# Performance work log

Hardware: AMD Instinct MI355X
Metric: run time of the kernel (lower is better)

## Reference

```python
import jax, jax.numpy as jnp
import numpy as np

N = 100000
E = 1600000
C_IN = 128
C_OUT = 128
EPS = 1e-5


def setup_inputs() -> dict:
    key = jax.random.key(0)
    ks = jax.random.split(key, 8)
    x = jax.random.normal(ks[0], (N, C_IN), dtype=jnp.float32)
    edge_index = jax.random.randint(ks[1], (2, E), 0, N, dtype=jnp.int64)
    s_proj = 1.0 / np.sqrt(C_IN)
    s_out = 1.0 / np.sqrt(C_IN)
    W_proj = jax.random.uniform(ks[2], (C_IN, C_IN), jnp.float32, -s_proj, s_proj)
    b_proj = jax.random.uniform(ks[3], (C_IN,), jnp.float32, -s_proj, s_proj)
    W_l = jax.random.uniform(ks[4], (C_OUT, C_IN), jnp.float32, -s_out, s_out)
    b_l = jax.random.uniform(ks[5], (C_OUT,), jnp.float32, -s_out, s_out)
    W_r = jax.random.uniform(ks[6], (C_OUT, C_IN), jnp.float32, -s_out, s_out)
    gamma = jnp.ones((C_OUT,), jnp.float32)
    beta = jnp.zeros((C_OUT,), jnp.float32)
    return {"x": x, "edge_index": edge_index, "W_proj": W_proj, "b_proj": b_proj,
            "W_l": W_l, "b_l": b_l, "W_r": W_r, "gamma": gamma, "beta": beta}


def reference(x, edge_index, W_proj, b_proj, W_l, b_l, W_r, gamma, beta):
    # SAGEConv(project=True, aggr='sum'): project+ReLU source features per node,
    # gather along edges, scatter-sum at targets, then lin_l(agg) + lin_r(x_root).
    src, dst = edge_index[0], edge_index[1]
    h = jax.nn.relu(x @ W_proj.T + b_proj)            # [N, C_IN]
    msg = h[src]                                       # [E, C_IN] edge gather
    agg = jax.ops.segment_sum(msg, dst, num_segments=N)  # [N, C_IN]
    out = agg @ W_l.T + b_l + x @ W_r.T                # [N, C_OUT] (root uses unprojected x)
    # LayerNorm(c_out)
    mu = jnp.mean(out, axis=-1, keepdims=True)
    var = jnp.var(out, axis=-1, keepdims=True)
    return (out - mu) * jax.lax.rsqrt(var + EPS) * gamma + beta
```

## Files before the change

### kernel.cpp

```cpp
#include <hip/hip_runtime.h>
#include <stdint.h>

#define NN 100000
#define NE 1600000
#define C  128
#define NB 782
#define CAP 4096
#define SB_SHIFT 13
#define MB 782

typedef __attribute__((ext_vector_type(8))) short short8;
typedef __attribute__((ext_vector_type(4))) float f32x4;

__device__ __forceinline__ float bf2f(uint16_t u) {
  union { uint32_t u; float f; } v; v.u = ((uint32_t)u) << 16; return v.f;
}
__device__ __forceinline__ uint16_t f2bf(float f) {
  union { float f; uint32_t u; } v; v.f = f;
  uint32_t r = v.u + 0x7fffu + ((v.u >> 16) & 1u);
  return (uint16_t)(r >> 16);
}

__global__ __launch_bounds__(256) void cast3_k(
    const float* __restrict__ a, const float* __restrict__ b, const float* __restrict__ c,
    uint16_t* __restrict__ oa, uint16_t* __restrict__ ob, uint16_t* __restrict__ oc)
{
  int i = blockIdx.x * 256 + threadIdx.x;
  int which = i >> 12, j = i & 4095;
  const float* s = which == 0 ? a : (which == 1 ? b : c);
  uint16_t* d    = which == 0 ? oa : (which == 1 ? ob : oc);
  float4 v = ((const float4*)s)[j];
  uint2 p;
  p.x = (uint32_t)f2bf(v.x) | ((uint32_t)f2bf(v.y) << 16);
  p.y = (uint32_t)f2bf(v.z) | ((uint32_t)f2bf(v.w) << 16);
  ((uint2*)d)[j] = p;
}


__global__ __launch_bounds__(512) void gemm_proj_k(
    const float* __restrict__ x, const uint16_t* __restrict__ wpb,
    const float* __restrict__ bias, uint16_t* __restrict__ h,
    uint16_t* __restrict__ xb)
{
  extern __shared__ uint8_t slds[];
  const int t = threadIdx.x;
#pragma unroll
  for (int q = 0; q < 4; ++q) {
    int ci = q * 512 + t;
    int c = ci >> 4, k16 = ci & 15;
    *(short8*)(slds + c * 256 + ((k16 ^ (c & 15)) << 4)) =
        *(const short8*)(wpb + ci * 8);
  }
  __syncthreads();

  const int w = t >> 6, lane = t & 63;
  const int tile_m = blockIdx.x * 128 + w * 16;
  if (tile_m >= NN) return;
  const int r16 = lane & 15, g = lane >> 4;

  short8 a[4];
  const float* xp = x + (size_t)(tile_m + r16) * C + g * 8;
  uint16_t* xbp = xb + (size_t)(tile_m + r16) * C + g * 8;
#pragma unroll
  for (int kk = 0; kk < 4; ++kk) {
    float4 u = *(const float4*)(xp + kk * 32);
    float4 v = *(const float4*)(xp + kk * 32 + 4);
    short8 av;
    av[0] = (short)f2bf(u.x); av[1] = (short)f2bf(u.y);
    av[2] = (short)f2bf(u.z); av[3] = (short)f2bf(u.w);
    av[4] = (short)f2bf(v.x); av[5] = (short)f2bf(v.y);
    av[6] = (short)f2bf(v.z); av[7] = (short)f2bf(v.w);
    a[kk] = av;
    *(short8*)(xbp + kk * 32) = av;
  }

#pragma unroll
  for (int nt = 0; nt < 8; ++nt) {
    f32x4 acc = {0.f, 0.f, 0.f, 0.f};
    const int c = nt * 16 + r16;
    const uint8_t* rb = slds + c * 256;
#pragma unroll
    for (int kk = 0; kk < 4; ++kk) {
      short8 b = *(const short8*)(rb + ((((kk << 2) + g) ^ (c & 15)) << 4));
      acc = __builtin_amdgcn_mfma_f32_16x16x32_bf16(a[kk], b, acc, 0, 0, 0);
    }
    const float bv = bias[c];
#pragma unroll
    for (int r = 0; r < 4; ++r) {
      int row = tile_m + g * 4 + r;
      float v = acc[r] + bv;
      v = v > 0.f ? v : 0.f;
      h[(size_t)row * C + c] = f2bf(v);
    }
  }
}

__global__ __launch_bounds__(256) void phase1_k(
    const int* __restrict__ esrc, const int* __restrict__ edst,
    int* __restrict__ gcnt, uint32_t* __restrict__ ebuf)
{
  __shared__ int bh[NB];
  __shared__ int gb[NB];
  const int t = threadIdx.x;
  const int base = blockIdx.x * 6400;

  for (int i = t; i < NB; i += 256) bh[i] = 0;

  const int4* ed4 = (const int4*)(edst + base);
  const int4* es4 = (const int4*)(esrc + base);
  int4 dv[6], sv[6];
#pragma unroll
  for (int i = 0; i < 6; ++i) { dv[i] = ed4[i * 256 + t]; sv[i] = es4[i * 256 + t]; }
  const int dlast = edst[base + 6144 + t];
  const int slast = esrc[base + 6144 + t];
  __syncthreads();

#pragma unroll
  for (int i = 0; i < 6; ++i) {
    atomicAdd(&bh[dv[i].x >> 7], 1); atomicAdd(&bh[dv[i].y >> 7], 1);
    atomicAdd(&bh[dv[i].z >> 7], 1); atomicAdd(&bh[dv[i].w >> 7], 1);
  }
  atomicAdd(&bh[dlast >> 7], 1);
  __syncthreads();

  for (int i = t; i < NB; i += 256) {
    int c = bh[i];
    gb[i] = c ? atomicAdd(&gcnt[i], c) : 0;
    bh[i] = 0;
  }
  __syncthreads();

#define P1_SCATTER(d, s) do { \
    int bb = (d) >> 7; \
    int o = atomicAdd(&bh[bb], 1); \
    int pos = gb[bb] + o; \
    if (pos < CAP) ebuf[(size_t)bb * CAP + pos] = ((uint32_t)((d) & 127) << 17) | (uint32_t)(s); \
  } while (0)

#pragma unroll
  for (int i = 0; i < 6; ++i) {
    P1_SCATTER(dv[i].x, sv[i].x); P1_SCATTER(dv[i].y, sv[i].y);
    P1_SCATTER(dv[i].z, sv[i].z); P1_SCATTER(dv[i].w, sv[i].w);
  }
  P1_SCATTER(dlast, slast);
#undef P1_SCATTER
}

__global__ __launch_bounds__(1024) void scan_block_k(
    const int* __restrict__ in, int* __restrict__ out, int n)
{
  __shared__ int sm[1024];
  int t = threadIdx.x;
  int v = (t < n) ? in[t] : 0;
  sm[t] = v;
  __syncthreads();
  for (int off = 1; off < 1024; off <<= 1) {
    int x = (t >= off) ? sm[t - off] : 0;
    __syncthreads();
    sm[t] += x;
    __syncthreads();
  }
  if (t < n) out[t] = sm[t] - v;
}

__global__ __launch_bounds__(256) void phase2_k(
    const uint32_t* __restrict__ ebuf, const int* __restrict__ gcnt,
    const int* __restrict__ gbase, int* __restrict__ ssrc,
    int* __restrict__ start, int* __restrict__ deg)
{
  __shared__ uint32_t raw[CAP];
  __shared__ int lout[CAP];
  __shared__ int cnt2[128 * 16];
  __shared__ int nd[128];
  const int b = blockIdx.x, t = threadIdx.x;
  const int n0 = b * 128;
  int cnt = gcnt[b]; if (cnt > CAP) cnt = CAP;
  const int base = gbase[b];

  for (int i = t; i < 128 * 16; i += 256) cnt2[i] = 0;
  __syncthreads();
  for (int i = t; i < cnt; i += 256) {
    uint32_t v = ebuf[(size_t)b * CAP + i];
    raw[i] = v;
    atomicAdd(&cnt2[(v >> 17) * 16 + ((v & 0x1FFFFu) >> SB_SHIFT)], 1);
  }
  __syncthreads();

  int deg_t = 0;
  if (t < 128) {
#pragma unroll
    for (int i = 0; i < 16; ++i) deg_t += cnt2[t * 16 + i];
    nd[t] = deg_t;
  }
  __syncthreads();
  for (int off = 1; off < 128; off <<= 1) {
    int v = 0;
    if (t < 128 && t >= off) v = nd[t - off];
    __syncthreads();
    if (t < 128) nd[t] += v;
    __syncthreads();
  }
  if (t < 128) {
    int pref = nd[t] - deg_t;
    if (n0 + t < NN) { start[n0 + t] = base + pref; deg[n0 + t] = deg_t; }
    int run = pref;
#pragma unroll
    for (int i = 0; i < 16; ++i) { int c = cnt2[t * 16 + i]; cnt2[t * 16 + i] = run; run += c; }
  }
  __syncthreads();
  for (int i = t; i < cnt; i += 256) {
    uint32_t v = raw[i];
    int o = atomicAdd(&cnt2[(v >> 17) * 16 + ((v & 0x1FFFFu) >> SB_SHIFT)], 1);
    lout[o] = (int)(v & 0x1FFFFu);
  }
  __syncthreads();
  for (int i = t; i < cnt; i += 256) ssrc[base + i] = lout[i];
}

__global__ __launch_bounds__(256) void aggregate_k(
    const uint16_t* __restrict__ h, const int* __restrict__ ssrc,
    const int* __restrict__ start, const int* __restrict__ deg,
    uint16_t* __restrict__ agg)
{
  const int wid = (blockIdx.x * 256 + threadIdx.x) >> 6;
  if (wid >= NN) return;
  const int lane = threadIdx.x & 63;
  const int half = lane >> 5;
  const int l32 = lane & 31;
  const int s0 = start[wid];
  const int cnt = deg[wid];
  const size_t choff = (size_t)l32 * 4;
  float a0 = 0.f, a1 = 0.f, a2 = 0.f, a3 = 0.f;

#define ACC(v) do { \
    a0 += bf2f((uint16_t)(v).x); a1 += bf2f((uint16_t)((v).x >> 16)); \
    a2 += bf2f((uint16_t)(v).y); a3 += bf2f((uint16_t)((v).y >> 16)); \
  } while (0)

  int j = 0;
  for (; j + 8 <= cnt; j += 8) {
    int e0 = ssrc[s0 + j + 0 + half];
    int e1 = ssrc[s0 + j + 2 + half];
    int e2 = ssrc[s0 + j + 4 + half];
    int e3 = ssrc[s0 + j + 6 + half];
    uint2 v0 = *(const uint2*)(h + (size_t)e0 * C + choff);
    uint2 v1 = *(const uint2*)(h + (size_t)e1 * C + choff);
    uint2 v2 = *(const uint2*)(h + (size_t)e2 * C + choff);
    uint2 v3 = *(const uint2*)(h + (size_t)e3 * C + choff);
    ACC(v0); ACC(v1); ACC(v2); ACC(v3);
  }
  for (; j + 2 <= cnt; j += 2) {
    int e = ssrc[s0 + j + half];
    uint2 v = *(const uint2*)(h + (size_t)e * C + choff);
    ACC(v);
  }
  if (j < cnt && half == 0) {
    int e = ssrc[s0 + j];
    uint2 v = *(const uint2*)(h + (size_t)e * C + choff);
    ACC(v);
  }
#undef ACC

  a0 += __shfl_xor(a0, 32, 64);
  a1 += __shfl_xor(a1, 32, 64);
  a2 += __shfl_xor(a2, 32, 64);
  a3 += __shfl_xor(a3, 32, 64);
  if (half == 0) {
    uint2 p;
    p.x = (uint32_t)f2bf(a0) | ((uint32_t)f2bf(a1) << 16);
    p.y = (uint32_t)f2bf(a2) | ((uint32_t)f2bf(a3) << 16);
    *(uint2*)(agg + (size_t)wid * C + choff) = p;
  }
}

__global__ __launch_bounds__(512) void gemm_out_k(
    const uint16_t* __restrict__ aggb, const uint16_t* __restrict__ xb,
    const uint16_t* __restrict__ wlb, const uint16_t* __restrict__ wrb,
    const float* __restrict__ bl, const float* __restrict__ gamma,
    const float* __restrict__ beta, float* __restrict__ out)
{
  extern __shared__ uint8_t slds[];
  const int t = threadIdx.x;
#pragma unroll
  for (int q = 0; q < 4; ++q) {
    int ci = q * 512 + t;
    int c = ci >> 4, k16 = ci & 15;
    *(short8*)(slds + c * 256 + ((k16 ^ (c & 15)) << 4)) =
        *(const short8*)(wlb + ci * 8);
  }
#pragma unroll
  for (int q = 0; q < 4; ++q) {
    int ci = q * 512 + t;
    int c = ci >> 4, k16 = ci & 15;
    *(short8*)(slds + 32768 + c * 256 + ((k16 ^ (c & 15)) << 4)) =
        *(const short8*)(wrb + ci * 8);
  }
  __syncthreads();

  const int w = t >> 6, lane = t & 63;
  const int tile_m = blockIdx.x * 128 + w * 16;
  if (tile_m >= NN) return;
  const int r16 = lane & 15, g = lane >> 4;

  short8 a0[4], a1[4];
  const uint16_t* p0 = aggb + (size_t)(tile_m + r16) * C + g * 8;
  const uint16_t* p1 = xb   + (size_t)(tile_m + r16) * C + g * 8;
#pragma unroll
  for (int kk = 0; kk < 4; ++kk) {
    a0[kk] = *(const short8*)(p0 + kk * 32);
    a1[kk] = *(const short8*)(p1 + kk * 32);
  }

  f32x4 acc[8];
#pragma unroll
  for (int nt = 0; nt < 8; ++nt) {
    f32x4 c4 = {0.f, 0.f, 0.f, 0.f};
    const int c = nt * 16 + r16;
    const uint8_t* rbl = slds + c * 256;
    const uint8_t* rbr = slds + 32768 + c * 256;
#pragma unroll
    for (int kk = 0; kk < 4; ++kk) {
      short8 b = *(const short8*)(rbl + ((((kk << 2) + g) ^ (c & 15)) << 4));
      c4 = __builtin_amdgcn_mfma_f32_16x16x32_bf16(a0[kk], b, c4, 0, 0, 0);
    }
#pragma unroll
    for (int kk = 0; kk < 4; ++kk) {
      short8 b = *(const short8*)(rbr + ((((kk << 2) + g) ^ (c & 15)) << 4));
      c4 = __builtin_amdgcn_mfma_f32_16x16x32_bf16(a1[kk], b, c4, 0, 0, 0);
    }
    const float bv = bl[c];
#pragma unroll
    for (int r = 0; r < 4; ++r) c4[r] += bv;
    acc[nt] = c4;
  }

  float s1[4], s2[4];
#pragma unroll
  for (int r = 0; r < 4; ++r) { s1[r] = 0.f; s2[r] = 0.f; }
#pragma unroll
  for (int nt = 0; nt < 8; ++nt)
#pragma unroll
    for (int r = 0; r < 4; ++r) { float v = acc[nt][r]; s1[r] += v; s2[r] += v * v; }
#pragma unroll
  for (int m = 1; m <= 8; m <<= 1) {
#pragma unroll
    for (int r = 0; r < 4; ++r) {
      s1[r] += __shfl_xor(s1[r], m, 64);
      s2[r] += __shfl_xor(s2[r], m, 64);
    }
  }
  float mean[4], rstd[4];
#pragma unroll
  for (int r = 0; r < 4; ++r) {
    mean[r] = s1[r] * (1.f / C);
    float var = s2[r] * (1.f / C) - mean[r] * mean[r];
    rstd[r] = rsqrtf(var + 1e-5f);
  }
#pragma unroll
  for (int nt = 0; nt < 8; ++nt) {
    const int col = nt * 16 + r16;
    const float gmv = gamma[col], btv = beta[col];
#pragma unroll
    for (int r = 0; r < 4; ++r) {
      int row = tile_m + g * 4 + r;
      out[(size_t)row * C + col] = (acc[nt][r] - mean[r]) * rstd[r] * gmv + btv;
    }
  }
}

extern "C" void kernel_launch(void* const* d_in, const int* in_sizes, int n_in,
                              void* d_out, int out_size, void* d_ws, size_t ws_size,
                              hipStream_t stream)
{
  const float* x        = (const float*)d_in[0];
  const int* ei         = (const int*)d_in[1];
  const float* Wp       = (const float*)d_in[2];
  const float* bp       = (const float*)d_in[3];
  const float* Wl       = (const float*)d_in[4];
  const float* bl       = (const float*)d_in[5];
  const float* Wr       = (const float*)d_in[6];
  const float* gamma    = (const float*)d_in[7];
  const float* beta     = (const float*)d_in[8];
  float* out            = (float*)d_out;

  char* ws = (char*)d_ws;
  uint16_t* xb   = (uint16_t*)(ws + 0);
  uint16_t* h    = (uint16_t*)(ws + 25600000);
  uint16_t* aggb = (uint16_t*)(ws + 51200000);
  uint32_t* ebuf = (uint32_t*)(ws + 51200000);
  uint16_t* wpb  = (uint16_t*)(ws + 76800000);
  uint16_t* wlb  = (uint16_t*)(ws + 76832768);
  uint16_t* wrb  = (uint16_t*)(ws + 76865536);
  int* deg       = (int*)(ws + 76898304);
  int* start     = (int*)(ws + 77298304);
  int* gcnt      = (int*)(ws + 77698304);
  int* gbase     = (int*)(ws + 77702400);
  int* ssrc      = (int*)(ws + 78102400);

  const int* esrc = ei;
  const int* edst = ei + NE;

  hipMemsetAsync(gcnt, 0, NB * sizeof(int), stream);

  cast3_k<<<48, 256, 0, stream>>>(Wp, Wl, Wr, wpb, wlb, wrb);
  gemm_proj_k<<<MB, 512, 32768, stream>>>(x, wpb, bp, h, xb);

  phase1_k<<<250, 256, 0, stream>>>(esrc, edst, gcnt, ebuf);
  scan_block_k<<<1, 1024, 0, stream>>>(gcnt, gbase, NB);
  phase2_k<<<NB, 256, 0, stream>>>(ebuf, gcnt, gbase, ssrc, start, deg);

  aggregate_k<<<(NN + 3) / 4, 256, 0, stream>>>(h, ssrc, start, deg, aggb);

  gemm_out_k<<<MB, 512, 65536, stream>>>(aggb, xb, wlb, wrb, bl, gamma, beta, out);
}
```

Baseline: 148.7 us.

## Fuse projection GEMM with edge bucketing pass and widen aggregate gathers

Merges the projection GEMM and the edge-bucketing phase1 kernel into a single launch. Block index selects which role a block plays, so the two independent jobs run concurrently and one launch is dropped. Phase1 blocks now use 512 threads and carve their histogram arrays out of dynamic shared memory. Separately, the aggregation kernel now has each lane read 16-byte chunks with four edges per wave step, plus a masked tail, to cut the number of gather instructions. The fused kernel risks occupancy limits from the larger shared-memory allocation applied to every block.

```diff
diff --git a/kernel.cpp b/kernel.cpp
--- a/kernel.cpp
+++ b/kernel.cpp
@@ -8,6 +8,7 @@
 #define CAP 4096
 #define SB_SHIFT 13
 #define MB 782
+#define P1B 250
 
 typedef __attribute__((ext_vector_type(8))) short short8;
 typedef __attribute__((ext_vector_type(4))) float f32x4;
@@ -37,113 +38,114 @@
 }
 
 
-__global__ __launch_bounds__(512) void gemm_proj_k(
+__global__ __launch_bounds__(512) void fused_front_k(
     const float* __restrict__ x, const uint16_t* __restrict__ wpb,
     const float* __restrict__ bias, uint16_t* __restrict__ h,
-    uint16_t* __restrict__ xb)
+    uint16_t* __restrict__ xb,
+    const int* __restrict__ esrc, const int* __restrict__ edst,
+    int* __restrict__ gcnt, uint32_t* __restrict__ ebuf)
 {
   extern __shared__ uint8_t slds[];
   const int t = threadIdx.x;
-#pragma unroll
-  for (int q = 0; q < 4; ++q) {
-    int ci = q * 512 + t;
-    int c = ci >> 4, k16 = ci & 15;
-    *(short8*)(slds + c * 256 + ((k16 ^ (c & 15)) << 4)) =
-        *(const short8*)(wpb + ci * 8);
-  }
-  __syncthreads();
-
-  const int w = t >> 6, lane = t & 63;
-  const int tile_m = blockIdx.x * 128 + w * 16;
-  if (tile_m >= NN) return;
-  const int r16 = lane & 15, g = lane >> 4;
-
-  short8 a[4];
-  const float* xp = x + (size_t)(tile_m + r16) * C + g * 8;
-  uint16_t* xbp = xb + (size_t)(tile_m + r16) * C + g * 8;
-#pragma unroll
-  for (int kk = 0; kk < 4; ++kk) {
-    float4 u = *(const float4*)(xp + kk * 32);
-    float4 v = *(const float4*)(xp + kk * 32 + 4);
-    short8 av;
-    av[0] = (short)f2bf(u.x); av[1] = (short)f2bf(u.y);
-    av[2] = (short)f2bf(u.z); av[3] = (short)f2bf(u.w);
-    av[4] = (short)f2bf(v.x); av[5] = (short)f2bf(v.y);
-    av[6] = (short)f2bf(v.z); av[7] = (short)f2bf(v.w);
-    a[kk] = av;
-    *(short8*)(xbp + kk * 32) = av;
-  }
-
-#pragma unroll
-  for (int nt = 0; nt < 8; ++nt) {
-    f32x4 acc = {0.f, 0.f, 0.f, 0.f};
-    const int c = nt * 16 + r16;
-    const uint8_t* rb = slds + c * 256;
+
+  if (blockIdx.x < MB) {
+#pragma unroll
+    for (int q = 0; q < 4; ++q) {
+      int ci = q * 512 + t;
+      int c = ci >> 4, k16 = ci & 15;
+      *(short8*)(slds + c * 256 + ((k16 ^ (c & 15)) << 4)) =
+          *(const short8*)(wpb + ci * 8);
+    }
+    __syncthreads();
+
+    const int w = t >> 6, lane = t & 63;
+    const int tile_m = blockIdx.x * 128 + w * 16;
+    if (tile_m >= NN) return;
+    const int r16 = lane & 15, g = lane >> 4;
+
+    short8 a[4];
+    const float* xp = x + (size_t)(tile_m + r16) * C + g * 8;
+    uint16_t* xbp = xb + (size_t)(tile_m + r16) * C + g * 8;
 #pragma unroll
     for (int kk = 0; kk < 4; ++kk) {
-      short8 b = *(const short8*)(rb + ((((kk << 2) + g) ^ (c & 15)) << 4));
-      acc = __builtin_amdgcn_mfma_f32_16x16x32_bf16(a[kk], b, acc, 0, 0, 0);
-    }
-    const float bv = bias[c];
-#pragma unroll
-    for (int r = 0; r < 4; ++r) {
-      int row = tile_m + g * 4 + r;
-      float v = acc[r] + bv;
-      v = v > 0.f ? v : 0.f;
-      h[(size_t)row * C + c] = f2bf(v);
-    }
-  }
-}
-
-__global__ __launch_bounds__(256) void phase1_k(
-    const int* __restrict__ esrc, const int* __restrict__ edst,
-    int* __restrict__ gcnt, uint32_t* __restrict__ ebuf)
-{
-  __shared__ int bh[NB];
-  __shared__ int gb[NB];
-  const int t = threadIdx.x;
-  const int base = blockIdx.x * 6400;
-
-  for (int i = t; i < NB; i += 256) bh[i] = 0;
-
-  const int4* ed4 = (const int4*)(edst + base);
-  const int4* es4 = (const int4*)(esrc + base);
-  int4 dv[6], sv[6];
-#pragma unroll
-  for (int i = 0; i < 6; ++i) { dv[i] = ed4[i * 256 + t]; sv[i] = es4[i * 256 + t]; }
-  const int dlast = edst[base + 6144 + t];
-  const int slast = esrc[base + 6144 + t];
-  __syncthreads();
-
-#pragma unroll
-  for (int i = 0; i < 6; ++i) {
-    atomicAdd(&bh[dv[i].x >> 7], 1); atomicAdd(&bh[dv[i].y >> 7], 1);
-    atomicAdd(&bh[dv[i].z >> 7], 1); atomicAdd(&bh[dv[i].w >> 7], 1);
-  }
-  atomicAdd(&bh[dlast >> 7], 1);
-  __syncthreads();
-
-  for (int i = t; i < NB; i += 256) {
-    int c = bh[i];
-    gb[i] = c ? atomicAdd(&gcnt[i], c) : 0;
-    bh[i] = 0;
-  }
-  __syncthreads();
+      float4 u = *(const float4*)(xp + kk * 32);
+      float4 v = *(const float4*)(xp + kk * 32 + 4);
+      short8 av;
+      av[0] = (short)f2bf(u.x); av[1] = (short)f2bf(u.y);
+      av[2] = (short)f2bf(u.z); av[3] = (short)f2bf(u.w);
+      av[4] = (short)f2bf(v.x); av[5] = (short)f2bf(v.y);
+      av[6] = (short)f2bf(v.z); av[7] = (short)f2bf(v.w);
+      a[kk] = av;
+      *(short8*)(xbp + kk * 32) = av;
+    }
+
+#pragma unroll
+    for (int nt = 0; nt < 8; ++nt) {
+      f32x4 acc = {0.f, 0.f, 0.f, 0.f};
+      const int c = nt * 16 + r16;
+      const uint8_t* rb = slds + c * 256;
+#pragma unroll
+      for (int kk = 0; kk < 4; ++kk) {
+        short8 b = *(const short8*)(rb + ((((kk << 2) + g) ^ (c & 15)) << 4));
+        acc = __builtin_amdgcn_mfma_f32_16x16x32_bf16(a[kk], b, acc, 0, 0, 0);
+      }
+      const float bv = bias[c];
+#pragma unroll
+      for (int r = 0; r < 4; ++r) {
+        int row = tile_m + g * 4 + r;
+        float v = acc[r] + bv;
+        v = v > 0.f ? v : 0.f;
+        h[(size_t)row * C + c] = f2bf(v);
+      }
+    }
+  } else {
+    int* bh = (int*)slds;
+    int* gb = bh + NB;
+    const int blk = blockIdx.x - MB;
+    const int base = blk * 6400;
+
+    for (int i = t; i < NB; i += 512) bh[i] = 0;
+
+    const int4* ed4 = (const int4*)(edst + base);
+    const int4* es4 = (const int4*)(esrc + base);
+    int4 dv[4], sv[4];
+    bool val[4];
+#pragma unroll
+    for (int k = 0; k < 4; ++k) {
+      int i = t + k * 512;
+      val[k] = (i < 1600);
+      if (val[k]) { dv[k] = ed4[i]; sv[k] = es4[i]; }
+    }
+    __syncthreads();
+
+#pragma unroll
+    for (int k = 0; k < 4; ++k) if (val[k]) {
+      atomicAdd(&bh[dv[k].x >> 7], 1); atomicAdd(&bh[dv[k].y >> 7], 1);
+      atomicAdd(&bh[dv[k].z >> 7], 1); atomicAdd(&bh[dv[k].w >> 7], 1);
+    }
+    __syncthreads();
+
+    for (int i = t; i < NB; i += 512) {
+      int c = bh[i];
+      gb[i] = c ? atomicAdd(&gcnt[i], c) : 0;
+      bh[i] = 0;
+    }
+    __syncthreads();
 
 #define P1_SCATTER(d, s) do { \
-    int bb = (d) >> 7; \
-    int o = atomicAdd(&bh[bb], 1); \
-    int pos = gb[bb] + o; \
-    if (pos < CAP) ebuf[(size_t)bb * CAP + pos] = ((uint32_t)((d) & 127) << 17) | (uint32_t)(s); \
-  } while (0)
-
-#pragma unroll
-  for (int i = 0; i < 6; ++i) {
-    P1_SCATTER(dv[i].x, sv[i].x); P1_SCATTER(dv[i].y, sv[i].y);
-    P1_SCATTER(dv[i].z, sv[i].z); P1_SCATTER(dv[i].w, sv[i].w);
-  }
-  P1_SCATTER(dlast, slast);
+      int bb = (d) >> 7; \
+      int o = atomicAdd(&bh[bb], 1); \
+      int pos = gb[bb] + o; \
+      if (pos < CAP) ebuf[(size_t)bb * CAP + pos] = ((uint32_t)((d) & 127) << 17) | (uint32_t)(s); \
+    } while (0)
+
+#pragma unroll
+    for (int k = 0; k < 4; ++k) if (val[k]) {
+      P1_SCATTER(dv[k].x, sv[k].x); P1_SCATTER(dv[k].y, sv[k].y);
+      P1_SCATTER(dv[k].z, sv[k].z); P1_SCATTER(dv[k].w, sv[k].w);
+    }
 #undef P1_SCATTER
+  }
 }
 
 __global__ __launch_bounds__(1024) void scan_block_k(
@@ -225,51 +227,67 @@
   const int wid = (blockIdx.x * 256 + threadIdx.x) >> 6;
   if (wid >= NN) return;
   const int lane = threadIdx.x & 63;
-  const int half = lane >> 5;
-  const int l32 = lane & 31;
+  const int q = lane >> 4;
+  const int l16 = lane & 15;
   const int s0 = start[wid];
   const int cnt = deg[wid];
-  const size_t choff = (size_t)l32 * 4;
-  float a0 = 0.f, a1 = 0.f, a2 = 0.f, a3 = 0.f;
-
-#define ACC(v) do { \
-    a0 += bf2f((uint16_t)(v).x); a1 += bf2f((uint16_t)((v).x >> 16)); \
-    a2 += bf2f((uint16_t)(v).y); a3 += bf2f((uint16_t)((v).y >> 16)); \
+  const size_t choff = (size_t)l16 * 8;
+  float a[8];
+#pragma unroll
+  for (int i = 0; i < 8; ++i) a[i] = 0.f;
+
+#define ACC8(v) do { \
+    a[0] += bf2f((uint16_t)(v).x); a[1] += bf2f((uint16_t)((v).x >> 16)); \
+    a[2] += bf2f((uint16_t)(v).y); a[3] += bf2f((uint16_t)((v).y >> 16)); \
+    a[4] += bf2f((uint16_t)(v).z); a[5] += bf2f((uint16_t)((v).z >> 16)); \
+    a[6] += bf2f((uint16_t)(v).w); a[7] += bf2f((uint16_t)((v).w >> 16)); \
   } while (0)
 
   int j = 0;
-  for (; j + 8 <= cnt; j += 8) {
-    int e0 = ssrc[s0 + j + 0 + half];
-    int e1 = ssrc[s0 + j + 2 + half];
-    int e2 = ssrc[s0 + j + 4 + half];
-    int e3 = ssrc[s0 + j + 6 + half];
-    uint2 v0 = *(const uint2*)(h + (size_t)e0 * C + choff);
-    uint2 v1 = *(const uint2*)(h + (size_t)e1 * C + choff);
-    uint2 v2 = *(const uint2*)(h + (size_t)e2 * C + choff);
-    uint2 v3 = *(const uint2*)(h + (size_t)e3 * C + choff);
-    ACC(v0); ACC(v1); ACC(v2); ACC(v3);
-  }
-  for (; j + 2 <= cnt; j += 2) {
-    int e = ssrc[s0 + j + half];
-    uint2 v = *(const uint2*)(h + (size_t)e * C + choff);
-    ACC(v);
-  }
-  if (j < cnt && half == 0) {
-    int e = ssrc[s0 + j];
-    uint2 v = *(const uint2*)(h + (size_t)e * C + choff);
-    ACC(v);
-  }
-#undef ACC
-
-  a0 += __shfl_xor(a0, 32, 64);
-  a1 += __shfl_xor(a1, 32, 64);
-  a2 += __shfl_xor(a2, 32, 64);
-  a3 += __shfl_xor(a3, 32, 64);
-  if (half == 0) {
-    uint2 p;
-    p.x = (uint32_t)f2bf(a0) | ((uint32_t)f2bf(a1) << 16);
-    p.y = (uint32_t)f2bf(a2) | ((uint32_t)f2bf(a3) << 16);
-    *(uint2*)(agg + (size_t)wid * C + choff) = p;
+  for (; j + 16 <= cnt; j += 16) {
+    int e0 = ssrc[s0 + j + q];
+    int e1 = ssrc[s0 + j + 4 + q];
+    int e2 = ssrc[s0 + j + 8 + q];
+    int e3 = ssrc[s0 + j + 12 + q];
+    uint4 v0 = *(const uint4*)(h + (size_t)e0 * C + choff);
+    uint4 v1 = *(const uint4*)(h + (size_t)e1 * C + choff);
+    uint4 v2 = *(const uint4*)(h + (size_t)e2 * C + choff);
+    uint4 v3 = *(const uint4*)(h + (size_t)e3 * C + choff);
+    ACC8(v0); ACC8(v1); ACC8(v2); ACC8(v3);
+  }
+  const int rem = cnt - j;
+  if (rem > 0) {
+    int i0 = (q      < rem) ? q      : 0;
+    int i1 = (q + 4  < rem) ? q + 4  : 0;
+    int i2 = (q + 8  < rem) ? q + 8  : 0;
+    int i3 = (q + 12 < rem) ? q + 12 : 0;
+    int e0 = ssrc[s0 + j + i0];
+    int e1 = ssrc[s0 + j + i1];
+    int e2 = ssrc[s0 + j + i2];
+    int e3 = ssrc[s0 + j + i3];
+    uint4 v0 = *(const uint4*)(h + (size_t)e0 * C + choff);
+    uint4 v1 = *(const uint4*)(h + (size_t)e1 * C + choff);
+    uint4 v2 = *(const uint4*)(h + (size_t)e2 * C + choff);
+    uint4 v3 = *(const uint4*)(h + (size_t)e3 * C + choff);
+    if (q < rem)      ACC8(v0);
+    if (q + 4 < rem)  ACC8(v1);
+    if (q + 8 < rem)  ACC8(v2);
+    if (q + 12 < rem) ACC8(v3);
+  }
+#undef ACC8
+
+#pragma unroll
+  for (int i = 0; i < 8; ++i) {
+    a[i] += __shfl_xor(a[i], 16, 64);
+    a[i] += __shfl_xor(a[i], 32, 64);
+  }
+  if (q == 0) {
+    uint4 p;
+    p.x = (uint32_t)f2bf(a[0]) | ((uint32_t)f2bf(a[1]) << 16);
+    p.y = (uint32_t)f2bf(a[2]) | ((uint32_t)f2bf(a[3]) << 16);
+    p.z = (uint32_t)f2bf(a[4]) | ((uint32_t)f2bf(a[5]) << 16);
+    p.w = (uint32_t)f2bf(a[6]) | ((uint32_t)f2bf(a[7]) << 16);
+    *(uint4*)(agg + (size_t)wid * C + choff) = p;
   }
 }
 
@@ -403,9 +421,10 @@
   hipMemsetAsync(gcnt, 0, NB * sizeof(int), stream);
 
   cast3_k<<<48, 256, 0, stream>>>(Wp, Wl, Wr, wpb, wlb, wrb);
-  gemm_proj_k<<<MB, 512, 32768, stream>>>(x, wpb, bp, h, xb);
-
-  phase1_k<<<250, 256, 0, stream>>>(esrc, edst, gcnt, ebuf);
+
+  fused_front_k<<<MB + P1B, 512, 32768, stream>>>(
+      x, wpb, bp, h, xb, esrc, edst, gcnt, ebuf);
+
   scan_block_k<<<1, 1024, 0, stream>>>(gcnt, gbase, NB);
   phase2_k<<<NB, 256, 0, stream>>>(ebuf, gcnt, gbase, ssrc, start, deg);
 
```

New measurement: 136.5 us. 1.09x faster.
